# Performance work log

Hardware: AMD Instinct MI355X
Metric: run time of the kernel (lower is better)

Reference implementation:

```python
import jax, jax.numpy as jnp
import numpy as np

NUM_HEADS = 4
GROUPS = 32
EPS = 1e-5


def group_norm(x, gamma, beta):
    B, C, H, W = x.shape
    xg = x.reshape(B, GROUPS, C // GROUPS, H, W)
    mu = xg.mean(axis=(2, 3, 4), keepdims=True)
    var = xg.var(axis=(2, 3, 4), keepdims=True)
    xg = (xg - mu) * jax.lax.rsqrt(var + EPS)
    return xg.reshape(B, C, H, W) * gamma[None, :, None, None] + beta[None, :, None, None]


def setup_inputs() -> dict:
    key = jax.random.key(0)
    ks = jax.random.split(key, 6)
    B, C, H, W = 16, 256, 32, 32
    x = jax.random.normal(ks[0], (B, C, H, W), dtype=jnp.float32)
    gn_gamma = jnp.ones((C,), dtype=jnp.float32)
    gn_beta = jnp.zeros((C,), dtype=jnp.float32)
    # 1x1 convs are pure channel GEMMs; store weights as [out_ch, in_ch]
    qkv_w = jax.random.normal(ks[1], (3 * C, C), dtype=jnp.float32) * (C ** -0.5)
    qkv_b = jnp.zeros((3 * C,), dtype=jnp.float32)
    # NOTE: original zero-inits proj; we use small random weights so the
    # attention path is exercised/testable (see notes).
    proj_w = jax.random.normal(ks[2], (C, C), dtype=jnp.float32) * 0.02
    proj_b = jnp.zeros((C,), dtype=jnp.float32)
    return {"x": x, "gn_gamma": gn_gamma, "gn_beta": gn_beta,
            "qkv_w": qkv_w, "qkv_b": qkv_b, "proj_w": proj_w, "proj_b": proj_b}


def reference(x, gn_gamma, gn_beta, qkv_w, qkv_b, proj_w, proj_b):
    B, C, H, W = x.shape
    N = H * W
    d = C // NUM_HEADS
    h = group_norm(x, gn_gamma, gn_beta)
    hf = h.reshape(B, C, N)  # [B, C, N]
    qkv = jnp.einsum('oc,bcn->bon', qkv_w, hf) + qkv_b[None, :, None]
    qkv = qkv.reshape(B, NUM_HEADS, 3 * d, N)
    q, k, v = jnp.split(qkv, 3, axis=2)  # each [B, h, d, N]
    scale = d ** -0.5
    attn = jax.nn.softmax(jnp.einsum('bhdn,bhdm->bhnm', q, k) * scale, axis=-1)
    out = jnp.einsum('bhnm,bhdm->bhdn', attn, v).reshape(B, C, N)
    out = jnp.einsum('oc,bcn->bon', proj_w, out) + proj_b[None, :, None]
    return x + out.reshape(B, C, H, W)
```

## Files before the change

kernel.cpp:

```cpp
#include <hip/hip_runtime.h>

typedef short bf16x8_t __attribute__((ext_vector_type(8)));
typedef float f32x4_t __attribute__((ext_vector_type(4)));

__device__ __forceinline__ float bf2f(unsigned short h) {
  union { unsigned int u; float f; } v; v.u = ((unsigned int)h) << 16; return v.f;
}
__device__ __forceinline__ unsigned short f2bf(float f) {
  union { float f; unsigned int u; } v; v.f = f;
  unsigned int u = v.u + 0x7FFFu + ((v.u >> 16) & 1u);
  return (unsigned short)(u >> 16);
}
__device__ __forceinline__ unsigned int fbits(float f) {
  return __builtin_bit_cast(unsigned int, f);
}
__device__ __forceinline__ float exp2_hw(float x) {
  return __builtin_amdgcn_exp2f(x);
}
__device__ __forceinline__ unsigned int pack_trunc(float lo, float hi) {
  return __builtin_amdgcn_perm(fbits(hi), fbits(lo), 0x07060302u);
}
__device__ __forceinline__ void gload_lds16(const void* gsrc, void* ldst) {
  __builtin_amdgcn_global_load_lds(
      (const __attribute__((address_space(1))) unsigned int*)gsrc,
      (__attribute__((address_space(3))) unsigned int*)ldst, 16, 0, 0);
}

__device__ __align__(16) unsigned short g_hT[16 * 1024 * 256];
__device__ __align__(16) unsigned short g_qT[16 * 4 * 1024 * 64];
__device__ __align__(16) unsigned short g_kT[16 * 4 * 1024 * 64];
__device__ __align__(16) unsigned short g_vN[16 * 4 * 64 * 1024];
__device__ __align__(16) unsigned short g_wq[768 * 256];
__device__ __align__(16) unsigned short g_wp[256 * 256];

__global__ __launch_bounds__(256) void gn_kernel(
    const float* __restrict__ x, const float* __restrict__ gamma,
    const float* __restrict__ beta, const float* __restrict__ qkv_w,
    const float* __restrict__ proj_w) {
  const int b = blockIdx.x >> 5, g = blockIdx.x & 31;
  const int t = threadIdx.x;
  const float4* xg = (const float4*)(x + (size_t)(b * 256 + g * 8) * 1024);

  __shared__ __align__(16) unsigned short lds[8192];
  __shared__ float red[16];

  float vals[32];
  float s = 0.f, sq = 0.f;
#pragma unroll
  for (int p = 0; p < 4; ++p) {
    int idx = t + p * 256;
    float4 a = xg[2 * idx], c = xg[2 * idx + 1];
    float tmp[8] = {a.x, a.y, a.z, a.w, c.x, c.y, c.z, c.w};
#pragma unroll
    for (int j = 0; j < 8; ++j) {
      vals[p * 8 + j] = tmp[j];
      s += tmp[j]; sq += tmp[j] * tmp[j];
    }
  }

  {
    int widx = (blockIdx.x * 256 + t) * 2;
    const float* wsrc;
    unsigned short* wdst;
    if (widx < 196608) { wsrc = qkv_w + widx; wdst = g_wq + widx; }
    else { wsrc = proj_w + (widx - 196608); wdst = g_wp + (widx - 196608); }
    float2 wv = *(const float2*)wsrc;
    wdst[0] = f2bf(wv.x); wdst[1] = f2bf(wv.y);
  }

#pragma unroll
  for (int m = 32; m; m >>= 1) {
    s += __shfl_xor(s, m, 64);
    sq += __shfl_xor(sq, m, 64);
  }
  const int w = t >> 6;
  if ((t & 63) == 0) { red[w] = s; red[8 + w] = sq; }
  __syncthreads();
  s = red[0] + red[1] + red[2] + red[3];
  sq = red[8] + red[9] + red[10] + red[11];
  const float mu = s * (1.f / 8192.f);
  const float var = sq * (1.f / 8192.f) - mu * mu;
  const float rstd = rsqrtf(var + 1e-5f);

#pragma unroll
  for (int p = 0; p < 4; ++p) {
    int idx = t + p * 256;
    int c = idx >> 7;
    float ga = gamma[g * 8 + c] * rstd;
    float be = beta[g * 8 + c] - mu * ga;
    union { unsigned short u[8]; uint4 v; } pk;
#pragma unroll
    for (int j = 0; j < 8; ++j) pk.u[j] = f2bf(vals[p * 8 + j] * ga + be);
    ((uint4*)lds)[idx] = pk.v;
  }
  __syncthreads();

  unsigned short* dstbase = g_hT + (size_t)b * 1024 * 256 + g * 8;
#pragma unroll
  for (int p = 0; p < 4; ++p) {
    int n = t + p * 256;
    union { unsigned short u[8]; uint4 v; } pk;
#pragma unroll
    for (int c = 0; c < 8; ++c) pk.u[c] = lds[c * 1024 + n];
    *(uint4*)(dstbase + (size_t)n * 256) = pk.v;
  }
}

template <int MODE>
__global__ __launch_bounds__(256, 2) void gemm_ct(
    const float* __restrict__ bias, const float* __restrict__ xres,
    float* __restrict__ outp) {
  constexpr int OT = (MODE == 0) ? 96 : 64;
  constexpr int NT = (MODE == 0) ? 256 : 128;
  constexpr int OI = OT / 16;
  constexpr int NJ = NT / 64;
  constexpr int ASL = OT * 8;
  constexpr int BSL = NT * 8;

  const int n0 = blockIdx.x * NT;
  const int oty = blockIdx.y, o0 = oty * OT;
  const int b = blockIdx.z;
  const int t = threadIdx.x;
  const int w = t >> 6, lane = t & 63, quad = lane >> 4, l15 = lane & 15;

  __shared__ uint4 as[ASL];
  __shared__ uint4 bs[BSL];

  const uint4* Bv = (const uint4*)g_hT;
  const unsigned short* Wb = (MODE == 0) ? g_wq : g_wp;

  f32x4_t acc[OI][NJ];
#pragma unroll
  for (int i = 0; i < OI; ++i)
#pragma unroll
    for (int j = 0; j < NJ; ++j) acc[i][j] = (f32x4_t){0.f, 0.f, 0.f, 0.f};

  for (int kb = 0; kb < 4; ++kb) {
#pragma unroll
    for (int p = 0; p < ASL / 256; ++p) {
      int L = p * 256 + t;
      int row = L >> 3, kc = (L & 7) ^ (row & 7);
      gload_lds16(Wb + (size_t)(o0 + row) * 256 + kb * 64 + kc * 8,
                  &as[p * 256 + w * 64]);
    }
#pragma unroll
    for (int p = 0; p < BSL / 256; ++p) {
      int L = p * 256 + t;
      int row = L >> 3, kc = (L & 7) ^ (row & 7);
      gload_lds16(&Bv[(size_t)(b * 1024 + n0 + row) * 32 + kb * 8 + kc],
                  &bs[p * 256 + w * 64]);
    }
    __syncthreads();
#pragma unroll
    for (int kk = 0; kk < 2; ++kk) {
      int ch = kk * 4 + quad;
      const int sw = ch ^ (l15 & 7);
      bf16x8_t af[OI];
#pragma unroll
      for (int i = 0; i < OI; ++i)
        af[i] = __builtin_bit_cast(bf16x8_t, as[(i * 16 + l15) * 8 + sw]);
#pragma unroll
      for (int j = 0; j < NJ; ++j) {
        bf16x8_t bf = __builtin_bit_cast(
            bf16x8_t, bs[(w * (NT / 4) + j * 16 + l15) * 8 + sw]);
#pragma unroll
        for (int i = 0; i < OI; ++i)
          acc[i][j] = __builtin_amdgcn_mfma_f32_16x16x32_bf16(af[i], bf, acc[i][j], 0, 0, 0);
      }
    }
    __syncthreads();
  }

  float bi[OI][4];
#pragma unroll
  for (int i = 0; i < OI; ++i)
#pragma unroll
    for (int r = 0; r < 4; ++r) bi[i][r] = bias[o0 + i * 16 + quad * 4 + r];

  if (MODE == 0) {
#pragma unroll
    for (int i = 0; i < OI; ++i) {
      const int r0 = o0 + i * 16;
      const int head = r0 / 192;
      const int win = r0 - head * 192;
      const int type = win >> 6;
      const int d0 = (win & 63) + quad * 4;
      if (type < 2) {
        const float sc = (type == 0) ? 0.18033688f : 1.0f;
        unsigned short* dst = (type == 0 ? g_qT : g_kT) + (size_t)(b * 4 + head) * 65536;
#pragma unroll
        for (int j = 0; j < NJ; ++j) {
          int n = n0 + w * 64 + j * 16 + l15;
          ushort4 pk;
          pk.x = f2bf((acc[i][j][0] + bi[i][0]) * sc);
          pk.y = f2bf((acc[i][j][1] + bi[i][1]) * sc);
          pk.z = f2bf((acc[i][j][2] + bi[i][2]) * sc);
          pk.w = f2bf((acc[i][j][3] + bi[i][3]) * sc);
          *(ushort4*)(dst + (size_t)n * 64 + d0) = pk;
        }
      } else {
        unsigned short* dst = g_vN + (size_t)(b * 4 + head) * 65536;
#pragma unroll
        for (int j = 0; j < NJ; ++j) {
          int n = n0 + w * 64 + j * 16 + l15;
#pragma unroll
          for (int r = 0; r < 4; ++r)
            dst[(size_t)(d0 + r) * 1024 + n] = f2bf(acc[i][j][r] + bi[i][r]);
        }
      }
    }
  } else {
#pragma unroll
    for (int i = 0; i < OI; ++i)
#pragma unroll
      for (int r = 0; r < 4; ++r) {
        int c = o0 + i * 16 + quad * 4 + r;
        const float* xr = xres + (((size_t)b * 256 + c) << 10);
        float* op = outp + (((size_t)b * 256 + c) << 10);
#pragma unroll
        for (int j = 0; j < NJ; ++j) {
          int n = n0 + w * 32 + j * 16 + l15;
          op[n] = acc[i][j][r] + bi[i][r] + xr[n];
        }
      }
  }
}

__global__ __launch_bounds__(256, 4) void attn_kernel() {
  const int bh = blockIdx.x;
  const int n0 = blockIdx.y * 64;
  const int t = threadIdx.x;
  const int w = t >> 6, lane = t & 63, quad = lane >> 4, l15 = lane & 15;
  const int b = bh >> 2, h = bh & 3;

  const uint4* qv = (const uint4*)(g_qT + (size_t)bh * 65536);
  const uint4* kv = (const uint4*)(g_kT + (size_t)bh * 65536);
  const uint4* vv = (const uint4*)(g_vN + (size_t)bh * 65536);

  __shared__ uint4 ks[512];
  __shared__ uint4 vs[512];
  __shared__ __align__(16) unsigned short Pt[4 * 16 * 72];

  uint4 qr[2];
#pragma unroll
  for (int kk = 0; kk < 2; ++kk)
    qr[kk] = qv[(size_t)(n0 + w * 16 + l15) * 8 + kk * 4 + quad];

  const int rr0 = t >> 3, cc = t & 7, rr1 = rr0 + 32;
  uint4 kr0 = kv[rr0 * 8 + cc], kr1 = kv[rr1 * 8 + cc];
  uint4 vr0 = vv[rr0 * 128 + cc], vr1 = vv[rr1 * 128 + cc];

  f32x4_t OA[4];
#pragma unroll
  for (int i = 0; i < 4; ++i) OA[i] = (f32x4_t){0.f, 0.f, 0.f, 0.f};
  float rsum = 0.f;

  unsigned short* Pw = Pt + w * 1152;

#pragma unroll 1
  for (int mt = 0; mt < 16; ++mt) {
    ks[cc * 64 + (rr0 ^ cc)] = kr0; ks[cc * 64 + (rr1 ^ cc)] = kr1;
    vs[cc * 64 + (rr0 ^ cc)] = vr0; vs[cc * 64 + (rr1 ^ cc)] = vr1;
    __syncthreads();

    if (mt < 15) {
      int m1 = (mt + 1) * 64;
      kr0 = kv[(m1 + rr0) * 8 + cc]; kr1 = kv[(m1 + rr1) * 8 + cc];
      vr0 = vv[rr0 * 128 + (mt + 1) * 8 + cc]; vr1 = vv[rr1 * 128 + (mt + 1) * 8 + cc];
    }

    f32x4_t sA[4];
#pragma unroll
    for (int i = 0; i < 4; ++i) sA[i] = (f32x4_t){0.f, 0.f, 0.f, 0.f};
#pragma unroll
    for (int kk = 0; kk < 2; ++kk) {
      int ch = kk * 4 + quad;
      bf16x8_t bq = __builtin_bit_cast(bf16x8_t, qr[kk]);
#pragma unroll
      for (int ms = 0; ms < 4; ++ms) {
        bf16x8_t ak = __builtin_bit_cast(bf16x8_t, ks[ch * 64 + ((ms * 16 + l15) ^ ch)]);
        sA[ms] = __builtin_amdgcn_mfma_f32_16x16x32_bf16(ak, bq, sA[ms], 0, 0, 0);
      }
    }

#pragma unroll
    for (int ms = 0; ms < 4; ++ms) {
      float a0 = exp2_hw(sA[ms][0]), a1 = exp2_hw(sA[ms][1]);
      float a2 = exp2_hw(sA[ms][2]), a3 = exp2_hw(sA[ms][3]);
      rsum += (a0 + a1) + (a2 + a3);
      uint2 pA;
      pA.x = pack_trunc(a0, a1);
      pA.y = pack_trunc(a2, a3);
      *(uint2*)(Pw + l15 * 72 + ms * 16 + quad * 4) = pA;
    }

#pragma unroll
    for (int km = 0; km < 2; ++km) {
      int ch = km * 4 + quad;
      bf16x8_t bp = *(const bf16x8_t*)(Pw + l15 * 72 + km * 32 + quad * 8);
#pragma unroll
      for (int ds = 0; ds < 4; ++ds) {
        bf16x8_t av = __builtin_bit_cast(bf16x8_t, vs[ch * 64 + ((ds * 16 + l15) ^ ch)]);
        OA[ds] = __builtin_amdgcn_mfma_f32_16x16x32_bf16(av, bp, OA[ds], 0, 0, 0);
      }
    }
    __syncthreads();
  }

  rsum += __shfl_xor(rsum, 16, 64);
  rsum += __shfl_xor(rsum, 32, 64);
  const float inv = 1.f / rsum;

  unsigned short* dstA = g_hT + ((size_t)b * 1024 + n0 + w * 16 + l15) * 256 + h * 64;
#pragma unroll
  for (int ds = 0; ds < 4; ++ds) {
    ushort4 pk;
    pk.x = f2bf(OA[ds][0] * inv); pk.y = f2bf(OA[ds][1] * inv);
    pk.z = f2bf(OA[ds][2] * inv); pk.w = f2bf(OA[ds][3] * inv);
    *(ushort4*)(dstA + ds * 16 + quad * 4) = pk;
  }
}

extern "C" void kernel_launch(void* const* d_in, const int* in_sizes, int n_in,
                              void* d_out, int out_size, void* d_ws, size_t ws_size,
                              hipStream_t stream) {
  const float* x = (const float*)d_in[0];
  const float* gam = (const float*)d_in[1];
  const float* bet = (const float*)d_in[2];
  const float* qkv_w = (const float*)d_in[3];
  const float* qkv_b = (const float*)d_in[4];
  const float* pr_w = (const float*)d_in[5];
  const float* pr_b = (const float*)d_in[6];
  float* out = (float*)d_out;

  gn_kernel<<<512, 256, 0, stream>>>(x, gam, bet, qkv_w, pr_w);
  gemm_ct<0><<<dim3(4, 8, 16), 256, 0, stream>>>(qkv_b, nullptr, nullptr);
  attn_kernel<<<dim3(64, 16), 256, 0, stream>>>();
  gemm_ct<1><<<dim3(8, 4, 16), 256, 0, stream>>>(pr_b, x, out);
}
```

Before: 140.9 us.

## Widen attention blocks to 8 waves and double-buffer K/V tiles in LDS

The attention kernel now runs 512 threads per block, covering 128 query rows instead of 64, so each K/V tile staged in LDS is reused by twice as many waves and the grid halves. K/V LDS tiles are double-buffered by iteration parity, which removes the trailing __syncthreads in each key-tile iteration. Each thread now loads one K and one V vector per tile instead of two. Larger blocks with launch bounds of 512 may lower occupancy and raise register pressure.

```diff
diff --git a/kernel.cpp b/kernel.cpp
--- a/kernel.cpp
+++ b/kernel.cpp
@@ -226,9 +226,9 @@
   }
 }
 
-__global__ __launch_bounds__(256, 4) void attn_kernel() {
+__global__ __launch_bounds__(512) void attn_kernel() {
   const int bh = blockIdx.x;
-  const int n0 = blockIdx.y * 64;
+  const int n0 = blockIdx.y * 128;
   const int t = threadIdx.x;
   const int w = t >> 6, lane = t & 63, quad = lane >> 4, l15 = lane & 15;
   const int b = bh >> 2, h = bh & 3;
@@ -237,18 +237,17 @@
   const uint4* kv = (const uint4*)(g_kT + (size_t)bh * 65536);
   const uint4* vv = (const uint4*)(g_vN + (size_t)bh * 65536);
 
-  __shared__ uint4 ks[512];
-  __shared__ uint4 vs[512];
-  __shared__ __align__(16) unsigned short Pt[4 * 16 * 72];
+  __shared__ uint4 ks[2][512];
+  __shared__ uint4 vs[2][512];
+  __shared__ __align__(16) unsigned short Pt[8 * 16 * 72];
 
   uint4 qr[2];
 #pragma unroll
   for (int kk = 0; kk < 2; ++kk)
     qr[kk] = qv[(size_t)(n0 + w * 16 + l15) * 8 + kk * 4 + quad];
 
-  const int rr0 = t >> 3, cc = t & 7, rr1 = rr0 + 32;
-  uint4 kr0 = kv[rr0 * 8 + cc], kr1 = kv[rr1 * 8 + cc];
-  uint4 vr0 = vv[rr0 * 128 + cc], vr1 = vv[rr1 * 128 + cc];
+  const int rr = t >> 3, cc = t & 7;
+  uint4 kr = kv[rr * 8 + cc], vr = vv[rr * 128 + cc];
 
   f32x4_t OA[4];
 #pragma unroll
@@ -259,14 +258,16 @@
 
 #pragma unroll 1
   for (int mt = 0; mt < 16; ++mt) {
-    ks[cc * 64 + (rr0 ^ cc)] = kr0; ks[cc * 64 + (rr1 ^ cc)] = kr1;
-    vs[cc * 64 + (rr0 ^ cc)] = vr0; vs[cc * 64 + (rr1 ^ cc)] = vr1;
+    uint4* kb = ks[mt & 1];
+    uint4* vb = vs[mt & 1];
+    kb[cc * 64 + (rr ^ cc)] = kr;
+    vb[cc * 64 + (rr ^ cc)] = vr;
     __syncthreads();
 
     if (mt < 15) {
       int m1 = (mt + 1) * 64;
-      kr0 = kv[(m1 + rr0) * 8 + cc]; kr1 = kv[(m1 + rr1) * 8 + cc];
-      vr0 = vv[rr0 * 128 + (mt + 1) * 8 + cc]; vr1 = vv[rr1 * 128 + (mt + 1) * 8 + cc];
+      kr = kv[(m1 + rr) * 8 + cc];
+      vr = vv[rr * 128 + (mt + 1) * 8 + cc];
     }
 
     f32x4_t sA[4];
@@ -278,7 +279,7 @@
       bf16x8_t bq = __builtin_bit_cast(bf16x8_t, qr[kk]);
 #pragma unroll
       for (int ms = 0; ms < 4; ++ms) {
-        bf16x8_t ak = __builtin_bit_cast(bf16x8_t, ks[ch * 64 + ((ms * 16 + l15) ^ ch)]);
+        bf16x8_t ak = __builtin_bit_cast(bf16x8_t, kb[ch * 64 + ((ms * 16 + l15) ^ ch)]);
         sA[ms] = __builtin_amdgcn_mfma_f32_16x16x32_bf16(ak, bq, sA[ms], 0, 0, 0);
       }
     }
@@ -300,24 +301,23 @@
       bf16x8_t bp = *(const bf16x8_t*)(Pw + l15 * 72 + km * 32 + quad * 8);
 #pragma unroll
       for (int ds = 0; ds < 4; ++ds) {
-        bf16x8_t av = __builtin_bit_cast(bf16x8_t, vs[ch * 64 + ((ds * 16 + l15) ^ ch)]);
+        bf16x8_t av = __builtin_bit_cast(bf16x8_t, vb[ch * 64 + ((ds * 16 + l15) ^ ch)]);
         OA[ds] = __builtin_amdgcn_mfma_f32_16x16x32_bf16(av, bp, OA[ds], 0, 0, 0);
       }
     }
-    __syncthreads();
   }
 
   rsum += __shfl_xor(rsum, 16, 64);
   rsum += __shfl_xor(rsum, 32, 64);
   const float inv = 1.f / rsum;
 
-  unsigned short* dstA = g_hT + ((size_t)b * 1024 + n0 + w * 16 + l15) * 256 + h * 64;
+  unsigned short* dst = g_hT + ((size_t)b * 1024 + n0 + w * 16 + l15) * 256 + h * 64;
 #pragma unroll
   for (int ds = 0; ds < 4; ++ds) {
     ushort4 pk;
     pk.x = f2bf(OA[ds][0] * inv); pk.y = f2bf(OA[ds][1] * inv);
     pk.z = f2bf(OA[ds][2] * inv); pk.w = f2bf(OA[ds][3] * inv);
-    *(ushort4*)(dstA + ds * 16 + quad * 4) = pk;
+    *(ushort4*)(dst + ds * 16 + quad * 4) = pk;
   }
 }
 
@@ -335,6 +335,6 @@
 
   gn_kernel<<<512, 256, 0, stream>>>(x, gam, bet, qkv_w, pr_w);
   gemm_ct<0><<<dim3(4, 8, 16), 256, 0, stream>>>(qkv_b, nullptr, nullptr);
-  attn_kernel<<<dim3(64, 16), 256, 0, stream>>>();
+  attn_kernel<<<dim3(64, 8), 512, 0, stream>>>();
   gemm_ct<1><<<dim3(8, 4, 16), 256, 0, stream>>>(pr_b, x, out);
 }
```

Measured after the change: 136.6 us. 1.03x faster.
